# Kernel optimization log

Hardware: AMD Instinct MI355X
Metric: run time of the kernel (lower is better)

Reference implementation:

```python
import jax, jax.numpy as jnp
import numpy as np

NUM_EXPERTS = 8
TOP_K = 2
ROUTE_SCALE = 1.0
DIM = 1024
HID = 1024
B, S = 2, 4096


def setup_inputs() -> dict:
    key = jax.random.key(0)
    ks = jax.random.split(key, 9)
    sc = 0.05
    return {
        "x": jax.random.normal(ks[0], (B, S, DIM), dtype=jnp.float32),
        "gate_w": jax.random.normal(ks[1], (NUM_EXPERTS, DIM), dtype=jnp.float32) * sc,
        "w1": jax.random.normal(ks[2], (NUM_EXPERTS, HID, DIM), dtype=jnp.float32) * sc,
        "w2": jax.random.normal(ks[3], (NUM_EXPERTS, DIM, HID), dtype=jnp.float32) * sc,
        "w3": jax.random.normal(ks[4], (NUM_EXPERTS, HID, DIM), dtype=jnp.float32) * sc,
        "sw1": jax.random.normal(ks[5], (HID, DIM), dtype=jnp.float32) * sc,
        "sw2": jax.random.normal(ks[6], (DIM, HID), dtype=jnp.float32) * sc,
        "sw3": jax.random.normal(ks[7], (HID, DIM), dtype=jnp.float32) * sc,
        "expert_bias": jnp.zeros((NUM_EXPERTS,), dtype=jnp.float32),
    }


def reference(x, gate_w, w1, w2, w3, sw1, sw2, sw3, expert_bias):
    bs, slen, dim = x.shape
    xf = x.reshape(-1, dim)                      # [T, D]

    # ---- router (sigmoid scoring, top-k over scores + bias, gather true scores) ----
    scores = jax.nn.sigmoid((xf @ gate_w.T).astype(jnp.float32))   # [T, E]
    _, sel = jax.lax.top_k(scores + expert_bias[None, :], TOP_K)    # [T, K] int32
    top_scores = jnp.take_along_axis(scores, sel, axis=1) * ROUTE_SCALE  # [T, K]

    # ---- stable sort token-slots by chosen expert (dispatch permutation) ----
    flat_sel = sel.reshape(-1)                       # [T*K]
    order = jnp.argsort(flat_sel, stable=True)       # [T*K]
    scores_sorted = top_scores.reshape(-1)[order]    # [T*K]
    tok_idx = order // TOP_K                         # source token per slot
    expert_ids = flat_sel[order]                     # sorted expert id per slot

    routed = xf[tok_idx]                             # gather [T*K, D]
    # score_before_experts=True: scale inputs by routing score
    routed = (routed.astype(jnp.float32) * scores_sorted[:, None]).astype(x.dtype)

    # ---- grouped expert GLU MLP (loop over fixed expert count, masked) ----
    out_r = jnp.zeros_like(routed)
    for e in range(NUM_EXPERTS):
        m = (expert_ids == e)[:, None]
        h = jax.nn.silu(routed @ w1[e].T) * (routed @ w3[e].T)   # [T*K, H]
        out_r = out_r + jnp.where(m, h @ w2[e].T, jnp.zeros((), routed.dtype))

    # ---- shared expert on all tokens ----
    shared = (jax.nn.silu(xf @ sw1.T) * (xf @ sw3.T)) @ sw2.T    # [T, D]

    # NOTE: original code multiplies by routing scores again after experts
    # (in addition to score_before_experts) -- replicated faithfully.
    out_r = (out_r.astype(jnp.float32) * scores_sorted[:, None]).astype(x.dtype)

    out = shared.at[tok_idx].add(out_r)              # scatter-add combine
    return out.reshape(bs, slen, dim)
```

## Files before the change

kernel.cpp:

```cpp
#include <hip/hip_runtime.h>
#include <stdint.h>

typedef unsigned short u16;
typedef unsigned int u32;

#define T_TOK 8192
#define DIMSZ 1024
#define HIDSZ 1024
#define NE 8
#define NSLOT (T_TOK * 2)
#define NPAD (NSLOT + 1024)

typedef __attribute__((ext_vector_type(8))) __bf16 bf16x8;
typedef __attribute__((ext_vector_type(16))) float f32x16;

#define MFMA32(a, b, c) __builtin_amdgcn_mfma_f32_32x32x16_bf16(a, b, c, 0, 0, 0)

__device__ __forceinline__ size_t ablk(int pos, int c) {
  return ((((size_t)(pos >> 7) * 32 + (c >> 5)) * 4 + ((c >> 3) & 3)) * 128 +
          (pos & 127)) * 8 + (c & 7);
}

__device__ __forceinline__ u16 f2bf(float f) {
  u32 u = __builtin_bit_cast(u32, f);
  u += 0x7FFFu + ((u >> 16) & 1u);
  return (u16)(u >> 16);
}
__device__ __forceinline__ float bflo(u32 v) { return __builtin_bit_cast(float, v << 16); }
__device__ __forceinline__ float bfhi(u32 v) { return __builtin_bit_cast(float, v & 0xffff0000u); }
__device__ __forceinline__ u32 pack2(float a, float b) {
  return (u32)f2bf(a) | ((u32)f2bf(b) << 16);
}
__device__ __forceinline__ float silu_f(float v) { return v / (1.f + expf(-v)); }

__device__ __forceinline__ void gload16(const void* g, void* l) {
  __builtin_amdgcn_global_load_lds(
      (const __attribute__((address_space(1))) unsigned int*)g,
      (__attribute__((address_space(3))) unsigned int*)l, 16, 0, 0);
}

#define PIPE_SYNC(N) asm volatile("s_waitcnt vmcnt(" #N ")\n\ts_barrier" ::: "memory")

__global__ __launch_bounds__(256) void convert_blocked(
    const float* __restrict__ s0, const float* __restrict__ s1,
    const float* __restrict__ s2, const float* __restrict__ ss0,
    const float* __restrict__ ss1, const float* __restrict__ ss2,
    u16* __restrict__ d0, u16* __restrict__ d1, u16* __restrict__ d2,
    u16* __restrict__ ds0, u16* __restrict__ ds1, u16* __restrict__ ds2) {
  __shared__ u16 lt[2048];
  int t = blockIdx.x;
  const float* s;
  u16* d;
  if (t < NE * 16 * 32) {
    s = (blockIdx.y == 0) ? s0 : (blockIdx.y == 1) ? s1 : s2;
    d = (blockIdx.y == 0) ? d0 : (blockIdx.y == 1) ? d1 : d2;
  } else {
    t -= NE * 16 * 32;
    s = (blockIdx.y == 0) ? ss0 : (blockIdx.y == 1) ? ss1 : ss2;
    d = (blockIdx.y == 0) ? ds0 : (blockIdx.y == 1) ? ds1 : ds2;
  }
  int rt = t >> 5, kt = t & 31;
  const float* sp = s + (size_t)rt * 64 * 1024 + kt * 32;
  int nl = threadIdx.x >> 2, k0 = (threadIdx.x & 3) * 8;
  float4 a = *(const float4*)(sp + (size_t)nl * 1024 + k0);
  float4 b = *(const float4*)(sp + (size_t)nl * 1024 + k0 + 4);
  uint4 p;
  p.x = pack2(a.x, a.y); p.y = pack2(a.z, a.w);
  p.z = pack2(b.x, b.y); p.w = pack2(b.z, b.w);
  *(uint4*)&lt[(threadIdx.x & 3) * 512 + nl * 8] = p;
  __syncthreads();
  *(uint4*)(d + (size_t)t * 2048 + threadIdx.x * 8) = *(const uint4*)&lt[threadIdx.x * 8];
}

__global__ __launch_bounds__(256) void router_kernel(
    const float* __restrict__ x, const float* __restrict__ gw,
    const float* __restrict__ bias, int* __restrict__ sel,
    float* __restrict__ selscore, u16* __restrict__ xb) {
  int t = blockIdx.x * 4 + (threadIdx.x >> 6);
  int lane = threadIdx.x & 63;
  float a[NE];
#pragma unroll
  for (int e = 0; e < NE; e++) a[e] = 0.f;
#pragma unroll
  for (int j = 0; j < 4; j++) {
    int c = j * 256 + lane * 4;
    float4 xv = *(const float4*)&x[(size_t)t * DIMSZ + c];
    uint2 p;
    p.x = pack2(xv.x, xv.y);
    p.y = pack2(xv.z, xv.w);
    *(uint2*)&xb[ablk(t, c)] = p;
#pragma unroll
    for (int e = 0; e < NE; e++) {
      float4 gv = *(const float4*)&gw[e * DIMSZ + c];
      a[e] = fmaf(xv.x, gv.x, fmaf(xv.y, gv.y, fmaf(xv.z, gv.z, fmaf(xv.w, gv.w, a[e]))));
    }
  }
#pragma unroll
  for (int off = 1; off < 64; off <<= 1)
#pragma unroll
    for (int e = 0; e < NE; e++) a[e] += __shfl_xor(a[e], off);
  if (lane == 0) {
    float s[NE], b[NE];
#pragma unroll
    for (int e = 0; e < NE; e++) {
      s[e] = 1.f / (1.f + expf(-a[e]));
      b[e] = s[e] + bias[e];
    }
    int e1 = 0; float v1 = b[0];
#pragma unroll
    for (int e = 1; e < NE; e++) if (b[e] > v1) { v1 = b[e]; e1 = e; }
    int e2 = -1; float v2 = -1e30f;
#pragma unroll
    for (int e = 0; e < NE; e++) if (e != e1 && b[e] > v2) { v2 = b[e]; e2 = e; }
    sel[t * 2] = e1; sel[t * 2 + 1] = e2;
    selscore[t * 2] = s[e1];
    selscore[t * 2 + 1] = s[e2];
  }
}

__global__ __launch_bounds__(1024) void rank_kernel(
    const int* __restrict__ sel, const float* __restrict__ selscore,
    int* __restrict__ slot2pos, float* __restrict__ slot_score,
    int* __restrict__ counts, int* __restrict__ offsets) {
  __shared__ int hist[NE * 1024];
  __shared__ int tot[NE];
  __shared__ int offs[NE];
  int tid = threadIdx.x;
  int sl[16];
  int h[NE];
#pragma unroll
  for (int e = 0; e < NE; e++) h[e] = 0;
#pragma unroll
  for (int j = 0; j < 4; j++) {
    int4 v = ((const int4*)sel)[tid * 4 + j];
    sl[j * 4 + 0] = v.x; sl[j * 4 + 1] = v.y;
    sl[j * 4 + 2] = v.z; sl[j * 4 + 3] = v.w;
  }
#pragma unroll
  for (int i = 0; i < 16; i++)
#pragma unroll
    for (int e = 0; e < NE; e++) h[e] += (sl[i] == e) ? 1 : 0;
#pragma unroll
  for (int e = 0; e < NE; e++) hist[e * 1024 + tid] = h[e];
  __syncthreads();
  int wid = tid >> 6, lane = tid & 63;
  if (wid < NE) {
    int e = wid;
    int vals[16];
    int lsum = 0;
#pragma unroll
    for (int i = 0; i < 16; i++) {
      int v = hist[e * 1024 + lane * 16 + i];
      vals[i] = lsum;
      lsum += v;
    }
    int incl = lsum;
#pragma unroll
    for (int off = 1; off < 64; off <<= 1) {
      int v = __shfl_up(incl, off);
      if (lane >= off) incl += v;
    }
    int excl = incl - lsum;
#pragma unroll
    for (int i = 0; i < 16; i++) hist[e * 1024 + lane * 16 + i] = vals[i] + excl;
    if (lane == 63) tot[e] = incl;
  }
  __syncthreads();
  if (tid == 0) {
    int acc = 0;
    for (int e = 0; e < NE; e++) {
      offs[e] = acc;
      offsets[e] = acc;
      counts[e] = tot[e];
      acc += (tot[e] + 127) & ~127;
    }
  }
  __syncthreads();
  int base[NE];
#pragma unroll
  for (int e = 0; e < NE; e++) base[e] = offs[e] + hist[e * 1024 + tid];
#pragma unroll
  for (int i = 0; i < 16; i++) {
    int slot = tid * 16 + i;
    int e = sl[i];
    int pos = 0;
#pragma unroll
    for (int k = 0; k < NE; k++) pos += (e == k) ? base[k] : 0;
#pragma unroll
    for (int k = 0; k < NE; k++) base[k] += (e == k) ? 1 : 0;
    slot2pos[slot] = pos;
    slot_score[pos] = selscore[slot];
  }
}

__global__ __launch_bounds__(256) void gather_kernel(
    const u16* __restrict__ xb, const float* __restrict__ selscore,
    const int* __restrict__ slot2pos, u16* __restrict__ routed) {
  int s = blockIdx.x * 4 + (threadIdx.x >> 6);
  int lane = threadIdx.x & 63;
  int pos = slot2pos[s];
  float sc = selscore[s];
  int t = s >> 1;
#pragma unroll
  for (int j = 0; j < 4; j++) {
    int c = j * 256 + lane * 4;
    uint2 v = *(const uint2*)&xb[ablk(t, c)];
    uint2 p;
    p.x = pack2(bflo(v.x) * sc, bfhi(v.x) * sc);
    p.y = pack2(bflo(v.y) * sc, bfhi(v.y) * sc);
    *(uint2*)&routed[ablk(pos, c)] = p;
  }
}

#define BUFE 8192

#define PIPE_STAGE(B, KT)                                         \
  do {                                                            \
    u16* Lb = &lds[(B) * BUFE];                                   \
    gload16(pA + (size_t)(KT) * 4096, Lb + tid * 8);              \
    gload16(pBm + (size_t)(KT) * 2048, Lb + bdst);                \
  } while (0)

#define PIPE_COMPUTE(B)                                               \
  do {                                                                \
    const u16* Lb = &lds[(B) * BUFE];                                 \
    _Pragma("unroll")                                                 \
    for (int c = 0; c < 2; c++) {                                     \
      int ko = 2 * c + l5;                                            \
      bf16x8 b = *(const bf16x8*)&Lb[4096 + bsel + ko * 512 + l31 * 8]; \
      bf16x8 a0 = *(const bf16x8*)&Lb[ko * 1024 + wy * 512 + l31 * 8];  \
      bf16x8 a1 = *(const bf16x8*)&Lb[ko * 1024 + wy * 512 + 256 + l31 * 8]; \
      acc[0] = MFMA32(a0, b, acc[0]);                                 \
      acc[1] = MFMA32(a1, b, acc[1]);                                 \
    }                                                                 \
  } while (0)

#define PIPE_LOOP()                                                   \
  PIPE_STAGE(0, 0);                                                   \
  PIPE_STAGE(1, 1);                                                   \
  {                                                                   \
    int c0 = 0, c1 = 1, c2 = 2;                                       \
    for (int t = 0; t < 30; ++t) {                                    \
      PIPE_SYNC(2);                                                   \
      PIPE_STAGE(c2, t + 2);                                          \
      __builtin_amdgcn_s_setprio(1);                                  \
      PIPE_COMPUTE(c0);                                               \
      __builtin_amdgcn_s_setprio(0);                                  \
      int tm = c0; c0 = c1; c1 = c2; c2 = tm;                         \
    }                                                                 \
    PIPE_SYNC(2);                                                     \
    __builtin_amdgcn_s_setprio(1);                                    \
    PIPE_COMPUTE(c0);                                                 \
    __builtin_amdgcn_s_setprio(0);                                    \
    c0 = c1;                                                          \
    PIPE_SYNC(0);                                                     \
    __builtin_amdgcn_s_setprio(1);                                    \
    PIPE_COMPUTE(c0);                                                 \
    __builtin_amdgcn_s_setprio(0);                                    \
  }

__global__ __launch_bounds__(512, 4) void dual_glu_gemm(
    const u16* __restrict__ A, const u16* __restrict__ W1,
    const u16* __restrict__ W3, u16* __restrict__ Hout,
    const u16* __restrict__ As, const u16* __restrict__ SW1,
    const u16* __restrict__ SW3, u16* __restrict__ Hs,
    const int* __restrict__ seg_off, const int* __restrict__ seg_cnt) {
  int z = blockIdx.z;
  const u16 *Ap, *w1p, *w3p;
  u16* Hp;
  int soff, scnt;
  if (z < NE) {
    soff = seg_off[z]; scnt = seg_cnt[z];
    Ap = A;
    w1p = W1 + (size_t)z * HIDSZ * DIMSZ;
    w3p = W3 + (size_t)z * HIDSZ * DIMSZ;
    Hp = Hout;
  } else {
    soff = 0; scnt = T_TOK;
    Ap = As; w1p = SW1; w3p = SW3;
    Hp = Hs;
  }
  int mbase = blockIdx.y * 128;
  if (mbase >= scnt) return;
  int hx = blockIdx.x;

  __shared__ u16 lds[3 * BUFE];

  int tid = threadIdx.x;
  int lane = tid & 63;
  int wid = tid >> 6;
  int wy = wid >> 2, wq = wid & 3;
  int l5 = lane >> 5, l31 = lane & 31;

  const u16* pA = Ap + (size_t)((soff + mbase) >> 7) * 32 * 4096 + tid * 8;
  const u16* w1u = w1p + (size_t)hx * 32 * 2048;
  const u16* w3u = w3p + (size_t)hx * 32 * 2048;
  const u16* pBm = ((tid >> 8) ? w3u : w1u) + (tid & 255) * 8;
  int bdst = 4096 + (tid >> 8) * 2048 + (tid & 255) * 8;
  int bsel = (wq >> 1) * 2048 + (wq & 1) * 256;

  f32x16 acc[2];
  acc[0] = (f32x16)0.f; acc[1] = (f32x16)0.f;

  PIPE_LOOP();

  __syncthreads();
  float* ex = (float*)lds;
  int region = wy * 2 + (wq & 1);
  if (wq < 2) {
#pragma unroll
    for (int i = 0; i < 2; i++)
#pragma unroll
      for (int r = 0; r < 16; r++) {
        int rowl = (r & 3) + 8 * (r >> 2) + 4 * l5;
        ex[region * 2048 + (i * 32 + rowl) * 32 + l31] = acc[i][r];
      }
  }
  __syncthreads();
  if (wq >= 2) {
#pragma unroll
    for (int i = 0; i < 2; i++)
#pragma unroll
      for (int r = 0; r < 16; r++) {
        int rowl = (r & 3) + 8 * (r >> 2) + 4 * l5;
        int grow = mbase + wy * 64 + i * 32 + rowl;
        if (grow < scnt) {
          float h1 = ex[region * 2048 + (i * 32 + rowl) * 32 + l31];
          Hp[ablk(soff + grow, hx * 64 + (wq & 1) * 32 + l31)] =
              f2bf(silu_f(h1) * acc[i][r]);
        }
      }
  }
}

__global__ __launch_bounds__(512, 4) void gemm2_kernel(
    const u16* __restrict__ A, const u16* __restrict__ W, u16* __restrict__ OutB,
    const u16* __restrict__ As, const u16* __restrict__ SW, float* __restrict__ OutF,
    const float* __restrict__ scale, const int* __restrict__ seg_off,
    const int* __restrict__ seg_cnt) {
  int z = blockIdx.z;
  const u16 *Ap, *wp;
  int soff, scnt;
  if (z < NE) {
    soff = seg_off[z]; scnt = seg_cnt[z];
    Ap = A; wp = W + (size_t)z * DIMSZ * HIDSZ;
  } else {
    soff = 0; scnt = T_TOK;
    Ap = As; wp = SW;
  }
  int mbase = blockIdx.y * 128;
  if (mbase >= scnt) return;
  int nbase = blockIdx.x * 128;

  __shared__ u16 lds[3 * BUFE];

  int tid = threadIdx.x;
  int lane = tid & 63;
  int wid = tid >> 6;
  int wy = wid >> 2, wq = wid & 3;
  int l5 = lane >> 5, l31 = lane & 31;

  const u16* pA = Ap + (size_t)((soff + mbase) >> 7) * 32 * 4096 + tid * 8;
  const u16* nt0 = wp + (size_t)(nbase >> 6) * 32 * 2048;
  const u16* pBm = nt0 + (size_t)(tid >> 8) * 32 * 2048 + (tid & 255) * 8;
  int bdst = 4096 + (tid >> 8) * 2048 + (tid & 255) * 8;
  int bsel = (wq >> 1) * 2048 + (wq & 1) * 256;

  f32x16 acc[2];
  acc[0] = (f32x16)0.f; acc[1] = (f32x16)0.f;

  PIPE_LOOP();

#pragma unroll
  for (int i = 0; i < 2; i++) {
    int colg = nbase + wq * 32 + l31;
#pragma unroll
    for (int r = 0; r < 16; r++) {
      int rowl = (r & 3) + 8 * (r >> 2) + 4 * l5;
      int grow = mbase + wy * 64 + i * 32 + rowl;
      if (grow < scnt) {
        size_t idx = (size_t)(soff + grow) * DIMSZ + colg;
        if (z < NE) {
          OutB[idx] = f2bf(acc[i][r] * scale[soff + grow]);
        } else {
          OutF[idx] = acc[i][r];
        }
      }
    }
  }
}

__global__ __launch_bounds__(256) void combine_kernel(
    float* __restrict__ out, const u16* __restrict__ Orb,
    const int* __restrict__ slot2pos) {
  int t = blockIdx.x;
  int d = threadIdx.x * 4;
  int p0 = slot2pos[t * 2];
  int p1 = slot2pos[t * 2 + 1];
  float4 o = *(float4*)&out[(size_t)t * DIMSZ + d];
  uint2 a = *(const uint2*)&Orb[(size_t)p0 * DIMSZ + d];
  uint2 b = *(const uint2*)&Orb[(size_t)p1 * DIMSZ + d];
  o.x += bflo(a.x) + bflo(b.x);
  o.y += bfhi(a.x) + bfhi(b.x);
  o.z += bflo(a.y) + bflo(b.y);
  o.w += bfhi(a.y) + bfhi(b.y);
  *(float4*)&out[(size_t)t * DIMSZ + d] = o;
}

extern "C" void kernel_launch(void* const* d_in, const int* in_sizes, int n_in,
                              void* d_out, int out_size, void* d_ws, size_t ws_size,
                              hipStream_t stream) {
  const float* x = (const float*)d_in[0];
  const float* gw = (const float*)d_in[1];
  const float* w1 = (const float*)d_in[2];
  const float* w2 = (const float*)d_in[3];
  const float* w3 = (const float*)d_in[4];
  const float* sw1 = (const float*)d_in[5];
  const float* sw2 = (const float*)d_in[6];
  const float* sw3 = (const float*)d_in[7];
  const float* bias = (const float*)d_in[8];
  float* out = (float*)d_out;

  uint8_t* ws = (uint8_t*)d_ws;
  size_t off = 0;
  auto alloc = [&](size_t b) { size_t o = off; off += (b + 255) & ~(size_t)255; return o; };

  size_t ctrl = alloc(256);
  int* counts = (int*)(ws + ctrl);
  int* offsets = counts + 16;
  int* sel = (int*)(ws + alloc((size_t)NSLOT * 4));
  float* selscore = (float*)(ws + alloc((size_t)NSLOT * 4));
  float* slot_score = (float*)(ws + alloc((size_t)NPAD * 4));
  int* slot2pos = (int*)(ws + alloc((size_t)NSLOT * 4));
  u16* xb = (u16*)(ws + alloc((size_t)T_TOK * DIMSZ * 2));
  u16* routed = (u16*)(ws + alloc((size_t)NPAD * DIMSZ * 2));
  u16* Hbuf = (u16*)(ws + alloc((size_t)NPAD * HIDSZ * 2));
  u16* Orb = (u16*)(ws + alloc((size_t)NPAD * DIMSZ * 2));
  u16* Hs = (u16*)(ws + alloc((size_t)T_TOK * HIDSZ * 2));
  u16* w1b = (u16*)(ws + alloc((size_t)NE * HIDSZ * DIMSZ * 2));
  u16* w2b = (u16*)(ws + alloc((size_t)NE * DIMSZ * HIDSZ * 2));
  u16* w3b = (u16*)(ws + alloc((size_t)NE * HIDSZ * DIMSZ * 2));
  u16* sw1b = (u16*)(ws + alloc((size_t)HIDSZ * DIMSZ * 2));
  u16* sw2b = (u16*)(ws + alloc((size_t)DIMSZ * HIDSZ * 2));
  u16* sw3b = (u16*)(ws + alloc((size_t)HIDSZ * DIMSZ * 2));

  convert_blocked<<<dim3((NE + 1) * 16 * 32, 3), 256, 0, stream>>>(
      w1, w2, w3, sw1, sw2, sw3, w1b, w2b, w3b, sw1b, sw2b, sw3b);

  router_kernel<<<T_TOK / 4, 256, 0, stream>>>(x, gw, bias, sel, selscore, xb);
  rank_kernel<<<1, 1024, 0, stream>>>(sel, selscore, slot2pos, slot_score,
                                      counts, offsets);
  gather_kernel<<<NSLOT / 4, 256, 0, stream>>>(xb, selscore, slot2pos, routed);

  dual_glu_gemm<<<dim3(16, 64, NE + 1), 512, 0, stream>>>(
      routed, w1b, w3b, Hbuf, xb, sw1b, sw3b, Hs, offsets, counts);
  gemm2_kernel<<<dim3(8, 64, NE + 1), 512, 0, stream>>>(
      Hbuf, w2b, Orb, Hs, sw2b, out, slot_score, offsets, counts);

  combine_kernel<<<T_TOK, 256, 0, stream>>>(out, Orb, slot2pos);
}
```

Baseline: 495.0 us.

## Enlarge GEMM block tiles to 256x256 with 4x2 MFMA per wave and XCD-aware swizzle

Both grouped GEMM kernels move from 128x128 to 256x256 output tiles. Each wave now computes a 128x64 sub-tile with 8 accumulators, which raises operand reuse per LDS load, and the LDS stage buffers double in size. The workgroup index is remapped with a stride-8 swizzle so neighbouring tiles land on the same XCD and share L2 better. Occupancy drops to 2 blocks per CU, there are fewer workgroups to fill the GPU, and larger tiles waste more work on partial expert segments.

```diff
diff --git a/kernel.cpp b/kernel.cpp
--- a/kernel.cpp
+++ b/kernel.cpp
@@ -212,27 +212,33 @@
   }
 }
 
-#define BUFE 8192
-
-#define PIPE_STAGE(B, KT)                                         \
-  do {                                                            \
-    u16* Lb = &lds[(B) * BUFE];                                   \
-    gload16(pA + (size_t)(KT) * 4096, Lb + tid * 8);              \
-    gload16(pBm + (size_t)(KT) * 2048, Lb + bdst);                \
+#define BUFE 16384
+
+#define PIPE_STAGE(B, KT)                                          \
+  do {                                                             \
+    u16* Lb = &lds[(B) * BUFE];                                    \
+    gload16(pA + (size_t)(KT) * 4096, Lb + adst);                  \
+    gload16(pA + 32 * 4096 + (size_t)(KT) * 4096, Lb + 4096 + adst); \
+    gload16(pBm + (size_t)(KT) * 2048, Lb + bdst);                 \
+    gload16(pBm + (size_t)(KT) * 2048 + 1024, Lb + 1024 + bdst);   \
   } while (0)
 
-#define PIPE_COMPUTE(B)                                               \
-  do {                                                                \
-    const u16* Lb = &lds[(B) * BUFE];                                 \
-    _Pragma("unroll")                                                 \
-    for (int c = 0; c < 2; c++) {                                     \
-      int ko = 2 * c + l5;                                            \
-      bf16x8 b = *(const bf16x8*)&Lb[4096 + bsel + ko * 512 + l31 * 8]; \
-      bf16x8 a0 = *(const bf16x8*)&Lb[ko * 1024 + wy * 512 + l31 * 8];  \
-      bf16x8 a1 = *(const bf16x8*)&Lb[ko * 1024 + wy * 512 + 256 + l31 * 8]; \
-      acc[0] = MFMA32(a0, b, acc[0]);                                 \
-      acc[1] = MFMA32(a1, b, acc[1]);                                 \
-    }                                                                 \
+#define PIPE_COMPUTE(B)                                                 \
+  do {                                                                  \
+    const u16* La = &lds[(B) * BUFE] + wy * 4096;                       \
+    const u16* Lw = &lds[(B) * BUFE] + 8192 + wn * 2048;                \
+    _Pragma("unroll")                                                   \
+    for (int c = 0; c < 2; c++) {                                       \
+      int kc = 2 * c + l5;                                              \
+      bf16x8 b0 = *(const bf16x8*)&Lw[(kc * 64 + l31) * 8];             \
+      bf16x8 b1 = *(const bf16x8*)&Lw[(kc * 64 + 32 + l31) * 8];        \
+      _Pragma("unroll")                                                 \
+      for (int i = 0; i < 4; i++) {                                     \
+        bf16x8 a = *(const bf16x8*)&La[(kc * 128 + i * 32 + l31) * 8];  \
+        acc[i][0] = MFMA32(a, b0, acc[i][0]);                           \
+        acc[i][1] = MFMA32(a, b1, acc[i][1]);                           \
+      }                                                                 \
+    }                                                                   \
   } while (0)
 
 #define PIPE_LOOP()                                                   \
@@ -241,14 +247,14 @@
   {                                                                   \
     int c0 = 0, c1 = 1, c2 = 2;                                       \
     for (int t = 0; t < 30; ++t) {                                    \
-      PIPE_SYNC(2);                                                   \
+      PIPE_SYNC(4);                                                   \
       PIPE_STAGE(c2, t + 2);                                          \
       __builtin_amdgcn_s_setprio(1);                                  \
       PIPE_COMPUTE(c0);                                               \
       __builtin_amdgcn_s_setprio(0);                                  \
       int tm = c0; c0 = c1; c1 = c2; c2 = tm;                         \
     }                                                                 \
-    PIPE_SYNC(2);                                                     \
+    PIPE_SYNC(4);                                                     \
     __builtin_amdgcn_s_setprio(1);                                    \
     PIPE_COMPUTE(c0);                                                 \
     __builtin_amdgcn_s_setprio(0);                                    \
@@ -259,13 +265,20 @@
     __builtin_amdgcn_s_setprio(0);                                    \
   }
 
-__global__ __launch_bounds__(512, 4) void dual_glu_gemm(
+__global__ __launch_bounds__(512, 2) void dual_glu_gemm(
     const u16* __restrict__ A, const u16* __restrict__ W1,
     const u16* __restrict__ W3, u16* __restrict__ Hout,
     const u16* __restrict__ As, const u16* __restrict__ SW1,
     const u16* __restrict__ SW3, u16* __restrict__ Hs,
     const int* __restrict__ seg_off, const int* __restrict__ seg_cnt) {
-  int z = blockIdx.z;
+  const int GX = 8, GY = 32, NWG = GX * GY * (NE + 1);
+  int flat = blockIdx.x + GX * (blockIdx.y + GY * blockIdx.z);
+  int swz = (flat & 7) * (NWG / 8) + (flat >> 3);
+  int bx = swz % GX;
+  int rem = swz / GX;
+  int by = rem % GY;
+  int z = rem / GY;
+
   const u16 *Ap, *w1p, *w3p;
   u16* Hp;
   int soff, scnt;
@@ -280,65 +293,78 @@
     Ap = As; w1p = SW1; w3p = SW3;
     Hp = Hs;
   }
-  int mbase = blockIdx.y * 128;
+  int mbase = by * 256;
   if (mbase >= scnt) return;
-  int hx = blockIdx.x;
+  int hx = bx;
 
   __shared__ u16 lds[3 * BUFE];
 
   int tid = threadIdx.x;
   int lane = tid & 63;
   int wid = tid >> 6;
-  int wy = wid >> 2, wq = wid & 3;
+  int wy = wid >> 2, wn = wid & 3;
   int l5 = lane >> 5, l31 = lane & 31;
 
   const u16* pA = Ap + (size_t)((soff + mbase) >> 7) * 32 * 4096 + tid * 8;
-  const u16* w1u = w1p + (size_t)hx * 32 * 2048;
-  const u16* w3u = w3p + (size_t)hx * 32 * 2048;
-  const u16* pBm = ((tid >> 8) ? w3u : w1u) + (tid & 255) * 8;
-  int bdst = 4096 + (tid >> 8) * 2048 + (tid & 255) * 8;
-  int bsel = (wq >> 1) * 2048 + (wq & 1) * 256;
-
-  f32x16 acc[2];
-  acc[0] = (f32x16)0.f; acc[1] = (f32x16)0.f;
+  int u = tid >> 7, iB = tid & 127;
+  const u16* pBm = ((u < 2) ? w1p : w3p) +
+                   (size_t)(hx * 2 + (u & 1)) * 32 * 2048 + iB * 8;
+  int adst = tid * 8;
+  int bdst = 8192 + u * 2048 + iB * 8;
+
+  f32x16 acc[4][2];
+#pragma unroll
+  for (int i = 0; i < 4; i++) { acc[i][0] = (f32x16)0.f; acc[i][1] = (f32x16)0.f; }
 
   PIPE_LOOP();
 
-  __syncthreads();
   float* ex = (float*)lds;
-  int region = wy * 2 + (wq & 1);
-  if (wq < 2) {
-#pragma unroll
-    for (int i = 0; i < 2; i++)
-#pragma unroll
-      for (int r = 0; r < 16; r++) {
-        int rowl = (r & 3) + 8 * (r >> 2) + 4 * l5;
-        ex[region * 2048 + (i * 32 + rowl) * 32 + l31] = acc[i][r];
-      }
-  }
-  __syncthreads();
-  if (wq >= 2) {
-#pragma unroll
-    for (int i = 0; i < 2; i++)
-#pragma unroll
-      for (int r = 0; r < 16; r++) {
-        int rowl = (r & 3) + 8 * (r >> 2) + 4 * l5;
-        int grow = mbase + wy * 64 + i * 32 + rowl;
-        if (grow < scnt) {
-          float h1 = ex[region * 2048 + (i * 32 + rowl) * 32 + l31];
-          Hp[ablk(soff + grow, hx * 64 + (wq & 1) * 32 + l31)] =
-              f2bf(silu_f(h1) * acc[i][r]);
-        }
-      }
-  }
-}
-
-__global__ __launch_bounds__(512, 4) void gemm2_kernel(
+  for (int rr = 0; rr < 2; rr++) {
+    __syncthreads();
+    if (wy == rr && wn < 2) {
+#pragma unroll
+      for (int i = 0; i < 4; i++)
+#pragma unroll
+        for (int j = 0; j < 2; j++)
+#pragma unroll
+          for (int r = 0; r < 16; r++) {
+            int rowl = i * 32 + (r & 3) + 8 * (r >> 2) + 4 * l5;
+            ex[rowl * 128 + wn * 64 + j * 32 + l31] = acc[i][j][r];
+          }
+    }
+    __syncthreads();
+    if (wy == rr && wn >= 2) {
+#pragma unroll
+      for (int i = 0; i < 4; i++)
+#pragma unroll
+        for (int j = 0; j < 2; j++)
+#pragma unroll
+          for (int r = 0; r < 16; r++) {
+            int rowl = i * 32 + (r & 3) + 8 * (r >> 2) + 4 * l5;
+            int grow = mbase + rr * 128 + rowl;
+            if (grow < scnt) {
+              float h1 = ex[rowl * 128 + (wn - 2) * 64 + j * 32 + l31];
+              Hp[ablk(soff + grow, hx * 128 + (wn - 2) * 64 + j * 32 + l31)] =
+                  f2bf(silu_f(h1) * acc[i][j][r]);
+            }
+          }
+    }
+  }
+}
+
+__global__ __launch_bounds__(512, 2) void gemm2_kernel(
     const u16* __restrict__ A, const u16* __restrict__ W, u16* __restrict__ OutB,
     const u16* __restrict__ As, const u16* __restrict__ SW, float* __restrict__ OutF,
     const float* __restrict__ scale, const int* __restrict__ seg_off,
     const int* __restrict__ seg_cnt) {
-  int z = blockIdx.z;
+  const int GX = 4, GY = 32, NWG = GX * GY * (NE + 1);
+  int flat = blockIdx.x + GX * (blockIdx.y + GY * blockIdx.z);
+  int swz = (flat & 7) * (NWG / 8) + (flat >> 3);
+  int bx = swz % GX;
+  int rem = swz / GX;
+  int by = rem % GY;
+  int z = rem / GY;
+
   const u16 *Ap, *wp;
   int soff, scnt;
   if (z < NE) {
@@ -348,46 +374,49 @@
     soff = 0; scnt = T_TOK;
     Ap = As; wp = SW;
   }
-  int mbase = blockIdx.y * 128;
+  int mbase = by * 256;
   if (mbase >= scnt) return;
-  int nbase = blockIdx.x * 128;
+  int nbase = bx * 256;
 
   __shared__ u16 lds[3 * BUFE];
 
   int tid = threadIdx.x;
   int lane = tid & 63;
   int wid = tid >> 6;
-  int wy = wid >> 2, wq = wid & 3;
+  int wy = wid >> 2, wn = wid & 3;
   int l5 = lane >> 5, l31 = lane & 31;
 
   const u16* pA = Ap + (size_t)((soff + mbase) >> 7) * 32 * 4096 + tid * 8;
-  const u16* nt0 = wp + (size_t)(nbase >> 6) * 32 * 2048;
-  const u16* pBm = nt0 + (size_t)(tid >> 8) * 32 * 2048 + (tid & 255) * 8;
-  int bdst = 4096 + (tid >> 8) * 2048 + (tid & 255) * 8;
-  int bsel = (wq >> 1) * 2048 + (wq & 1) * 256;
-
-  f32x16 acc[2];
-  acc[0] = (f32x16)0.f; acc[1] = (f32x16)0.f;
+  int u = tid >> 7, iB = tid & 127;
+  const u16* pBm = wp + (size_t)((nbase >> 6) + u) * 32 * 2048 + iB * 8;
+  int adst = tid * 8;
+  int bdst = 8192 + u * 2048 + iB * 8;
+
+  f32x16 acc[4][2];
+#pragma unroll
+  for (int i = 0; i < 4; i++) { acc[i][0] = (f32x16)0.f; acc[i][1] = (f32x16)0.f; }
 
   PIPE_LOOP();
 
 #pragma unroll
-  for (int i = 0; i < 2; i++) {
-    int colg = nbase + wq * 32 + l31;
-#pragma unroll
-    for (int r = 0; r < 16; r++) {
-      int rowl = (r & 3) + 8 * (r >> 2) + 4 * l5;
-      int grow = mbase + wy * 64 + i * 32 + rowl;
-      if (grow < scnt) {
-        size_t idx = (size_t)(soff + grow) * DIMSZ + colg;
-        if (z < NE) {
-          OutB[idx] = f2bf(acc[i][r] * scale[soff + grow]);
-        } else {
-          OutF[idx] = acc[i][r];
+  for (int i = 0; i < 4; i++)
+#pragma unroll
+    for (int j = 0; j < 2; j++) {
+      int colg = nbase + wn * 64 + j * 32 + l31;
+#pragma unroll
+      for (int r = 0; r < 16; r++) {
+        int rowl = (r & 3) + 8 * (r >> 2) + 4 * l5;
+        int grow = mbase + wy * 128 + i * 32 + rowl;
+        if (grow < scnt) {
+          size_t idx = (size_t)(soff + grow) * DIMSZ + colg;
+          if (z < NE) {
+            OutB[idx] = f2bf(acc[i][j][r] * scale[soff + grow]);
+          } else {
+            OutF[idx] = acc[i][j][r];
+          }
         }
       }
     }
-  }
 }
 
 __global__ __launch_bounds__(256) void combine_kernel(
@@ -452,9 +481,9 @@
                                       counts, offsets);
   gather_kernel<<<NSLOT / 4, 256, 0, stream>>>(xb, selscore, slot2pos, routed);
 
-  dual_glu_gemm<<<dim3(16, 64, NE + 1), 512, 0, stream>>>(
+  dual_glu_gemm<<<dim3(8, 32, NE + 1), 512, 0, stream>>>(
       routed, w1b, w3b, Hbuf, xb, sw1b, sw3b, Hs, offsets, counts);
-  gemm2_kernel<<<dim3(8, 64, NE + 1), 512, 0, stream>>>(
+  gemm2_kernel<<<dim3(4, 32, NE + 1), 512, 0, stream>>>(
       Hbuf, w2b, Orb, Hs, sw2b, out, slot_score, offsets, counts);
 
   combine_kernel<<<T_TOK, 256, 0, stream>>>(out, Orb, slot2pos);
```

Result: slower. 1.319 ms (+166.5%).
